# Performance work log

Measured on AMD Instinct MI355X. Metric: run time of the kernel, lower is better.

## Reference

```python
import jax, jax.numpy as jnp
import numpy as np

B, T, V, H, L = 128, 512, 96, 512, 3  # batch, seq_len, n_tokens, n_hidden, n_layers


def setup_inputs() -> dict:
    key = jax.random.key(0)
    ks = jax.random.split(key, 16)
    k = 1.0 / np.sqrt(H)  # PyTorch LSTM/Linear uniform init bound

    def u(kk, shape):
        return jax.random.uniform(kk, shape, jnp.float32, -k, k)

    return {
        "x": jax.random.normal(ks[0], (B, T, V), jnp.float32),
        "h0": jnp.zeros((L, B, H), jnp.float32),
        "c0": jnp.zeros((L, B, H), jnp.float32),
        # layer 0 (input dim V), layers 1-2 (input dim H); gate order i,f,g,o
        "W_ih0": u(ks[1], (4 * H, V)), "W_hh0": u(ks[2], (4 * H, H)),
        "b_ih0": u(ks[3], (4 * H,)), "b_hh0": u(ks[4], (4 * H,)),
        "W_ih1": u(ks[5], (4 * H, H)), "W_hh1": u(ks[6], (4 * H, H)),
        "b_ih1": u(ks[7], (4 * H,)), "b_hh1": u(ks[8], (4 * H,)),
        "W_ih2": u(ks[9], (4 * H, H)), "W_hh2": u(ks[10], (4 * H, H)),
        "b_ih2": u(ks[11], (4 * H,)), "b_hh2": u(ks[12], (4 * H,)),
        "W_fc": u(ks[13], (V, H)), "b_fc": u(ks[14], (V,)),
    }


def _lstm_layer(x, h0, c0, W_ih, W_hh, b_ih, b_hh):
    # Precompute input-to-gate GEMM for the whole sequence: [B,T,4H]
    xg = jnp.einsum('btd,gd->btg', x, W_ih) + b_ih + b_hh

    def step(carry, xg_t):
        h, c = carry
        g = xg_t + h @ W_hh.T  # [B,4H]
        i, f, gg, o = jnp.split(g, 4, axis=-1)
        c = jax.nn.sigmoid(f) * c + jax.nn.sigmoid(i) * jnp.tanh(gg)
        h = jax.nn.sigmoid(o) * jnp.tanh(c)
        return (h, c), h

    (hT, cT), ys = jax.lax.scan(step, (h0, c0), jnp.swapaxes(xg, 0, 1))
    return jnp.swapaxes(ys, 0, 1), hT, cT  # [B,T,H], [B,H], [B,H]


def reference(x, h0, c0, W_ih0, W_hh0, b_ih0, b_hh0, W_ih1, W_hh1, b_ih1, b_hh1,
              W_ih2, W_hh2, b_ih2, b_hh2, W_fc, b_fc):
    params = [(W_ih0, W_hh0, b_ih0, b_hh0),
              (W_ih1, W_hh1, b_ih1, b_hh1),
              (W_ih2, W_hh2, b_ih2, b_hh2)]
    out = x
    hs, cs = [], []
    for l, (Wi, Wh, bi, bh) in enumerate(params):
        out, hT, cT = _lstm_layer(out, h0[l], c0[l], Wi, Wh, bi, bh)
        hs.append(hT)
        cs.append(cT)
    # dropout (inter-layer and post-LSTM) is identity in eval/deterministic mode
    logits = jnp.einsum('bth,vh->btv', out, W_fc) + b_fc  # [B,T,V]
    return logits.reshape(-1, V), jnp.stack(hs), jnp.stack(cs)
```

## Files before the change

### kernel.cpp

```cpp
#include <hip/hip_runtime.h>

#define Bb 128
#define Tt 512
#define Vv 96
#define Hh 512
#define OUT_H 6291456
#define OUT_C 6488064

typedef _Float16 f16x4 __attribute__((ext_vector_type(4)));
typedef _Float16 f16x8 __attribute__((ext_vector_type(8)));
typedef float f32x4 __attribute__((ext_vector_type(4)));

struct KP {
  const float *x, *h0, *c0;
  const float *Wih0, *Whh0, *bih0, *bhh0;
  const float *Wih1, *Whh1, *bih1, *bhh1;
  const float *Wih2, *Whh2, *bih2, *bhh2;
  const float *Wfc, *bfc;
  float* out;
  unsigned* flags;
  float* fbias;
  _Float16* wimg;
  _Float16* wfc;
  _Float16* xb;
  _Float16* hbuf;
};

__device__ __forceinline__ float sigf(float x) { return 1.f / (1.f + __expf(-x)); }

__device__ __forceinline__ void st_dc_u32(unsigned* p, unsigned v) {
  __hip_atomic_store(p, v, __ATOMIC_RELAXED, __HIP_MEMORY_SCOPE_AGENT);
}

__device__ __forceinline__ void wait2(unsigned* flags, int w1, int t1, int w2, int t2) {
  unsigned* p1 = flags + w1;
  unsigned* p2 = flags + w2;
  int g = 0;
  for (;;) {
    int v1 = (int)__hip_atomic_load(p1, __ATOMIC_RELAXED, __HIP_MEMORY_SCOPE_AGENT);
    int v2 = (int)__hip_atomic_load(p2, __ATOMIC_RELAXED, __HIP_MEMORY_SCOPE_AGENT);
    if (__all(v1 >= t1 && v2 >= t2)) break;
    if (++g > 30000) break;
    if (g < 64) __builtin_amdgcn_s_sleep(2);
    else        __builtin_amdgcn_s_sleep(8);
  }
}

template <int KS>
__device__ __forceinline__ void load_pl(const _Float16* __restrict__ p, f16x4 (&av)[KS]) {
#pragma unroll
  for (int i = 0; i < KS; ++i) av[i] = *(const f16x4*)(p + i * 16);
}

template <int KS, int NF>
__device__ __forceinline__ void mma_swz(const f16x4 (&av)[KS], const _Float16* ldsb,
                                        int kb, int l15, int l4, f32x4 (&acc)[NF]) {
#pragma unroll
  for (int i = 0; i < KS; ++i) {
#pragma unroll
    for (int n = 0; n < NF; ++n) {
      const int gr = n * 16 + l15;
      const int idx = ((gr << 9) + kb + i * 16 + (l4 << 2)) ^ ((gr & 7) << 3);
      f16x4 bv = *(const f16x4*)(ldsb + idx);
      acc[n] = __builtin_amdgcn_mfma_f32_16x16x16f16(av[i], bv, acc[n], 0, 0, 0);
    }
  }
}

__global__ __launch_bounds__(256) void prologue_kernel(KP A) {
  const int tid = threadIdx.x, bid = blockIdx.x;
  const int gt = bid * 256 + tid, gn = 98 * 256;
  for (int i = gt; i < Bb * Tt * Vv; i += gn) A.xb[i] = (_Float16)A.x[i];
  for (int i = gt; i < 3 * Bb * Hh; i += gn) {
    int l = i >> 16, b = (i >> 9) & 127, col = i & 511;
    int half = b >> 6, bl = b & 63;
    A.hbuf[(size_t)((l * 2 + half) * 32 + 31) * 32768 + bl * 512 + col] = (_Float16)A.h0[i];
  }
  for (int i = gt; i < 3 * 2048; i += gn) {
    int l = i >> 11, cc = i & 2047;
    const float* bi = (l == 0) ? A.bih0 : (l == 1) ? A.bih1 : A.bih2;
    const float* bh = (l == 0) ? A.bhh0 : (l == 1) ? A.bhh1 : A.bhh2;
    A.fbias[i] = bi[cc] + bh[cc];
  }
  for (int i = gt; i < Vv; i += gn) A.fbias[3 * 2048 + i] = A.bfc[i];

  if (bid < 96) {
    const int l = bid >> 5, c = bid & 31;
    _Float16* img = A.wimg + (size_t)bid * 65536;
    const float* Wh = (l == 0) ? A.Whh0 : (l == 1) ? A.Whh1 : A.Whh2;
    for (int e = tid; e < 64 * 512; e += 256) {
      int r = e >> 9, k = e & 511;
      float v = Wh[((r >> 4) * 512 + c * 16 + (r & 15)) * Hh + k];
      img[(r * 512 + k) ^ ((r & 7) << 3)] = (_Float16)v;
    }
    if (l == 0) {
      for (int e = tid; e < 64 * 96; e += 256) {
        int r = e / 96, k = e - r * 96;
        img[32768 + r * 112 + k] = (_Float16)A.Wih0[((r >> 4) * 512 + c * 16 + (r & 15)) * Vv + k];
      }
    } else {
      const float* Wi = (l == 1) ? A.Wih1 : A.Wih2;
      for (int e = tid; e < 64 * 512; e += 256) {
        int r = e >> 9, k = e & 511;
        float v = Wi[((r >> 4) * 512 + c * 16 + (r & 15)) * Hh + k];
        img[32768 + ((r * 512 + k) ^ ((r & 7) << 3))] = (_Float16)v;
      }
    }
  } else {
    const int r0 = (bid - 96) * 48;
    for (int e = tid; e < 48 * 512; e += 256) {
      int r = r0 + (e >> 9), k = e & 511;
      A.wfc[(r * 512 + k) ^ ((r & 7) << 3)] = (_Float16)A.Wfc[r * 512 + k];
    }
  }
}

__global__ __launch_bounds__(512, 2) void lstm_persist(KP A) {
  __shared__ _Float16 wlds[65536];
  __shared__ float redx[6144];
  const int tid = threadIdx.x, bid = blockIdx.x;
  const int lane = tid & 63, w = tid >> 6;
  const int l15 = lane & 15, l4 = lane >> 4;
  const int mf = w & 3, kh = w >> 2;
  unsigned* flags = A.flags;

  __builtin_amdgcn_fence(__ATOMIC_ACQUIRE, "agent");

  const bool isfc = (bid >= 192);
  const int l = isfc ? 2 : (bid >> 6);
  const int half = isfc ? (bid - 192) : ((bid >> 5) & 1);
  const int c = isfc ? 0 : (bid & 31);
  const int grp = isfc ? 6 : (l * 2 + half);

  {
    const f16x8* src = isfc ? (const f16x8*)A.wfc
                            : (const f16x8*)(A.wimg + (size_t)(l * 32 + c) * 65536);
    f16x8* dst = (f16x8*)wlds;
    const int cnt = isfc ? 6144 : 8192;
    for (int e = tid; e < cnt; e += 512) dst[e] = src[e];
  }

  int w1, w2, off1, off2;
  if (!isfc) {
    w1 = grp * 32 + (lane & 31); off1 = 0;
    if (lane < 32) {
      if (l > 0) { w2 = (grp - 2) * 32 + lane; off2 = 1; }
      else       { w2 = w1; off2 = 0; }
    } else {
      if (l < 2) { w2 = (grp + 2) * 32 + (lane - 32); off2 = -31; }
      else       { w2 = 6 * 32 + half; off2 = -31; }
    }
  } else {
    w1 = (4 + half) * 32 + (lane & 31); off1 = 1;
    w2 = w1; off2 = 1;
  }

  const int arow = mf * 16 + l15;
  const int kb = kh * 256;

  if (!isfc) {
    float biasr[4], creg[4];
#pragma unroll
    for (int n = 0; n < 4; ++n) biasr[n] = A.fbias[l * 2048 + n * 512 + c * 16 + l15];
#pragma unroll
    for (int q = 0; q < 4; ++q)
      creg[q] = A.c0[(size_t)l * 65536 + (half * 64 + mf * 16 + (l4 << 2) + q) * 512 + c * 16 + l15];
    __syncthreads();

    for (int t = 0; t < Tt; ++t) {
      if (tid < 64) wait2(flags, w1, t + off1, w2, t + off2);
      __syncthreads();

      const _Float16* hpv = A.hbuf + (size_t)(grp * 32 + ((t - 1) & 31)) * 32768
                            + arow * 512 + kb + (l4 << 2);
      f32x4 acc[4] = {};
      if (l == 0) {
        f16x4 a2[16];
        load_pl<16>(hpv, a2);
        f16x4 ax[3];
        const _Float16* xp = A.xb + ((size_t)(half * 64 + arow) * 512 + t) * 96
                             + kh * 48 + (l4 << 2);
#pragma unroll
        for (int i = 0; i < 3; ++i) ax[i] = *(const f16x4*)(xp + i * 16);
#pragma unroll
        for (int i = 0; i < 3; ++i)
#pragma unroll
          for (int n = 0; n < 4; ++n) {
            const int gr = n * 16 + l15;
            f16x4 bv = *(const f16x4*)(wlds + 32768 + gr * 112 + kh * 48 + i * 16 + (l4 << 2));
            acc[n] = __builtin_amdgcn_mfma_f32_16x16x16f16(ax[i], bv, acc[n], 0, 0, 0);
          }
        mma_swz<16, 4>(a2, wlds, kb, l15, l4, acc);
      } else {
        const _Float16* hin = A.hbuf + (size_t)((grp - 2) * 32 + (t & 31)) * 32768
                              + arow * 512 + kb + (l4 << 2);
        f16x4 a1[16], a2[16];
        load_pl<16>(hin, a1);
        load_pl<16>(hpv, a2);
        mma_swz<16, 4>(a1, wlds + 32768, kb, l15, l4, acc);
        mma_swz<16, 4>(a2, wlds, kb, l15, l4, acc);
      }

      if (kh == 1) {
#pragma unroll
        for (int n = 0; n < 4; ++n)
          *(f32x4*)&redx[(mf * 4 + n) * 256 + l15 * 16 + (l4 << 2)] = acc[n];
      }
      __syncthreads();
      if (kh == 0) {
#pragma unroll
        for (int n = 0; n < 4; ++n)
          acc[n] += *(const f32x4*)&redx[(mf * 4 + n) * 256 + l15 * 16 + (l4 << 2)];
        _Float16* rp = A.hbuf + (size_t)(grp * 32 + (t & 31)) * 32768;
#pragma unroll
        for (int q = 0; q < 4; ++q) {
          const int bl = mf * 16 + (l4 << 2) + q;
          float gi = acc[0][q] + biasr[0];
          float gf = acc[1][q] + biasr[1];
          float gg = acc[2][q] + biasr[2];
          float go = acc[3][q] + biasr[3];
          float iv = sigf(gi), fv = sigf(gf), gv = tanhf(gg), ov = sigf(go);
          float cn = fv * creg[q] + iv * gv;
          creg[q] = cn;
          float hv = ov * tanhf(cn);
          union { _Float16 h; unsigned short u; } cvt; cvt.h = (_Float16)hv;
          unsigned hb = cvt.u, ob = (unsigned)__shfl_xor((int)hb, 1, 64);
          if ((l15 & 1) == 0)
            st_dc_u32((unsigned*)(rp + bl * 512 + c * 16 + l15), hb | (ob << 16));
          if (t == Tt - 1) {
            A.out[OUT_H + (l * Bb + half * 64 + bl) * 512 + c * 16 + l15] = hv;
            A.out[OUT_C + (l * Bb + half * 64 + bl) * 512 + c * 16 + l15] = cn;
          }
        }
      }
      __syncthreads();
      if (tid == 0) st_dc_u32(&flags[grp * 32 + c], (unsigned)(t + 1));
    }
  } else {
    float biasr[6];
#pragma unroll
    for (int n = 0; n < 6; ++n) biasr[n] = A.fbias[6144 + n * 16 + l15];
    __syncthreads();

    for (int t = 0; t < Tt; ++t) {
      if (tid < 64) wait2(flags, w1, t + off1, w2, t + off2);
      __syncthreads();

      const _Float16* hv2 = A.hbuf + (size_t)((4 + half) * 32 + (t & 31)) * 32768
                            + arow * 512 + kb + (l4 << 2);
      f16x4 a1[16];
      load_pl<16>(hv2, a1);
      f32x4 acc[6] = {};
      mma_swz<16, 6>(a1, wlds, kb, l15, l4, acc);

      if (kh == 1) {
#pragma unroll
        for (int n = 0; n < 6; ++n)
          *(f32x4*)&redx[(mf * 6 + n) * 256 + l15 * 16 + (l4 << 2)] = acc[n];
      }
      __syncthreads();
      if (kh == 0) {
#pragma unroll
        for (int n = 0; n < 6; ++n)
          acc[n] += *(const f32x4*)&redx[(mf * 6 + n) * 256 + l15 * 16 + (l4 << 2)];
#pragma unroll
        for (int q = 0; q < 4; ++q) {
          const int b = half * 64 + mf * 16 + (l4 << 2) + q;
#pragma unroll
          for (int n = 0; n < 6; ++n)
            A.out[((size_t)b * 512 + t) * 96 + n * 16 + l15] = acc[n][q] + biasr[n];
        }
      }
      __syncthreads();
      if (tid == 0) st_dc_u32(&flags[6 * 32 + half], (unsigned)(t + 1));
    }
  }
}

extern "C" void kernel_launch(void* const* d_in, const int* in_sizes, int n_in,
                              void* d_out, int out_size, void* d_ws, size_t ws_size,
                              hipStream_t stream) {
  char* base = (char*)d_ws;
  KP a;
  a.x    = (const float*)d_in[0];
  a.h0   = (const float*)d_in[1];
  a.c0   = (const float*)d_in[2];
  a.Wih0 = (const float*)d_in[3];  a.Whh0 = (const float*)d_in[4];
  a.bih0 = (const float*)d_in[5];  a.bhh0 = (const float*)d_in[6];
  a.Wih1 = (const float*)d_in[7];  a.Whh1 = (const float*)d_in[8];
  a.bih1 = (const float*)d_in[9];  a.bhh1 = (const float*)d_in[10];
  a.Wih2 = (const float*)d_in[11]; a.Whh2 = (const float*)d_in[12];
  a.bih2 = (const float*)d_in[13]; a.bhh2 = (const float*)d_in[14];
  a.Wfc  = (const float*)d_in[15]; a.bfc  = (const float*)d_in[16];
  a.out  = (float*)d_out;
  a.flags = (unsigned*)base;
  a.fbias = (float*)(base + 1024);
  a.wimg  = (_Float16*)(base + 26624);
  a.wfc   = (_Float16*)(base + 12609536);
  a.xb    = (_Float16*)(base + 12707840);
  a.hbuf  = (_Float16*)(base + 25290752);

  hipError_t err = hipMemsetAsync(a.flags, 0, 1024, stream);
  (void)err;
  hipLaunchKernelGGL(prologue_kernel, dim3(98), dim3(256), 0, stream, a);
  hipLaunchKernelGGL(lstm_persist, dim3(194), dim3(512), 0, stream, a);
}
```

Measured before the change: 5.766 ms.

## Retile recurrent MFMA work to 2x2 warp tiles with new LDS swizzle

```diff
diff --git a/kernel.cpp b/kernel.cpp
--- a/kernel.cpp
+++ b/kernel.cpp
@@ -42,27 +42,32 @@
     if (__all(v1 >= t1 && v2 >= t2)) break;
     if (++g > 30000) break;
     if (g < 64) __builtin_amdgcn_s_sleep(2);
-    else        __builtin_amdgcn_s_sleep(8);
+    else        __builtin_amdgcn_s_sleep(4);
   }
 }
 
 template <int KS>
-__device__ __forceinline__ void load_pl(const _Float16* __restrict__ p, f16x4 (&av)[KS]) {
-#pragma unroll
-  for (int i = 0; i < KS; ++i) av[i] = *(const f16x4*)(p + i * 16);
+__device__ __forceinline__ void load2(const _Float16* __restrict__ p, f16x4 (&av)[2][KS]) {
+#pragma unroll
+  for (int m = 0; m < 2; ++m)
+#pragma unroll
+    for (int i = 0; i < KS; ++i)
+      av[m][i] = *(const f16x4*)(p + m * 16 * 512 + i * 16);
 }
 
 template <int KS, int NF>
-__device__ __forceinline__ void mma_swz(const f16x4 (&av)[KS], const _Float16* ldsb,
-                                        int kb, int l15, int l4, f32x4 (&acc)[NF]) {
+__device__ __forceinline__ void mma2(const f16x4 (&av)[2][KS], const _Float16* ldsb,
+                                     int kb, int nbase, int l15, int l4,
+                                     f32x4 (&acc)[2][NF]) {
 #pragma unroll
   for (int i = 0; i < KS; ++i) {
 #pragma unroll
     for (int n = 0; n < NF; ++n) {
-      const int gr = n * 16 + l15;
-      const int idx = ((gr << 9) + kb + i * 16 + (l4 << 2)) ^ ((gr & 7) << 3);
+      const int gr = (nbase + n) * 16 + l15;
+      const int idx = ((gr << 9) + kb + i * 16 + (l4 << 2)) ^ ((gr & 15) << 2);
       f16x4 bv = *(const f16x4*)(ldsb + idx);
-      acc[n] = __builtin_amdgcn_mfma_f32_16x16x16f16(av[i], bv, acc[n], 0, 0, 0);
+      acc[0][n] = __builtin_amdgcn_mfma_f32_16x16x16f16(av[0][i], bv, acc[0][n], 0, 0, 0);
+      acc[1][n] = __builtin_amdgcn_mfma_f32_16x16x16f16(av[1][i], bv, acc[1][n], 0, 0, 0);
     }
   }
 }
@@ -91,7 +96,7 @@
     for (int e = tid; e < 64 * 512; e += 256) {
       int r = e >> 9, k = e & 511;
       float v = Wh[((r >> 4) * 512 + c * 16 + (r & 15)) * Hh + k];
-      img[(r * 512 + k) ^ ((r & 7) << 3)] = (_Float16)v;
+      img[(r * 512 + k) ^ ((r & 15) << 2)] = (_Float16)v;
     }
     if (l == 0) {
       for (int e = tid; e < 64 * 96; e += 256) {
@@ -103,14 +108,14 @@
       for (int e = tid; e < 64 * 512; e += 256) {
         int r = e >> 9, k = e & 511;
         float v = Wi[((r >> 4) * 512 + c * 16 + (r & 15)) * Hh + k];
-        img[32768 + ((r * 512 + k) ^ ((r & 7) << 3))] = (_Float16)v;
+        img[32768 + ((r * 512 + k) ^ ((r & 15) << 2))] = (_Float16)v;
       }
     }
   } else {
     const int r0 = (bid - 96) * 48;
     for (int e = tid; e < 48 * 512; e += 256) {
       int r = r0 + (e >> 9), k = e & 511;
-      A.wfc[(r * 512 + k) ^ ((r & 7) << 3)] = (_Float16)A.Wfc[r * 512 + k];
+      A.wfc[(r * 512 + k) ^ ((r & 15) << 2)] = (_Float16)A.Wfc[r * 512 + k];
     }
   }
 }
@@ -121,7 +126,7 @@
   const int tid = threadIdx.x, bid = blockIdx.x;
   const int lane = tid & 63, w = tid >> 6;
   const int l15 = lane & 15, l4 = lane >> 4;
-  const int mf = w & 3, kh = w >> 2;
+  const int mf = w & 1, nf = (w >> 1) & 1, kh = w >> 2;
   unsigned* flags = A.flags;
 
   __builtin_amdgcn_fence(__ATOMIC_ACQUIRE, "agent");
@@ -155,121 +160,155 @@
     w2 = w1; off2 = 1;
   }
 
-  const int arow = mf * 16 + l15;
   const int kb = kh * 256;
+  const int abase = (mf * 32 + l15) * 512 + kb + (l4 << 2);
 
   if (!isfc) {
-    float biasr[4], creg[4];
+    float biasr[4];
 #pragma unroll
     for (int n = 0; n < 4; ++n) biasr[n] = A.fbias[l * 2048 + n * 512 + c * 16 + l15];
-#pragma unroll
-    for (int q = 0; q < 4; ++q)
-      creg[q] = A.c0[(size_t)l * 65536 + (half * 64 + mf * 16 + (l4 << 2) + q) * 512 + c * 16 + l15];
+    float creg[2][4];
+    if (w < 2) {
+#pragma unroll
+      for (int m = 0; m < 2; ++m)
+#pragma unroll
+        for (int q = 0; q < 4; ++q)
+          creg[m][q] = A.c0[(size_t)l * 65536 + (half * 64 + mf * 32 + m * 16 + (l4 << 2) + q) * 512 + c * 16 + l15];
+    }
     __syncthreads();
 
     for (int t = 0; t < Tt; ++t) {
       if (tid < 64) wait2(flags, w1, t + off1, w2, t + off2);
       __syncthreads();
 
-      const _Float16* hpv = A.hbuf + (size_t)(grp * 32 + ((t - 1) & 31)) * 32768
-                            + arow * 512 + kb + (l4 << 2);
-      f32x4 acc[4] = {};
+      const _Float16* hpv = A.hbuf + (size_t)(grp * 32 + ((t - 1) & 31)) * 32768 + abase;
+      f32x4 acc[2][2] = {};
       if (l == 0) {
-        f16x4 a2[16];
-        load_pl<16>(hpv, a2);
-        f16x4 ax[3];
-        const _Float16* xp = A.xb + ((size_t)(half * 64 + arow) * 512 + t) * 96
-                             + kh * 48 + (l4 << 2);
-#pragma unroll
-        for (int i = 0; i < 3; ++i) ax[i] = *(const f16x4*)(xp + i * 16);
+        f16x4 ah[2][16];
+        load2<16>(hpv, ah);
+        f16x4 ax[2][3];
+#pragma unroll
+        for (int m = 0; m < 2; ++m) {
+          const _Float16* xp = A.xb + ((size_t)(half * 64 + mf * 32 + m * 16 + l15) * 512 + t) * 96
+                               + kh * 48 + (l4 << 2);
+#pragma unroll
+          for (int i = 0; i < 3; ++i) ax[m][i] = *(const f16x4*)(xp + i * 16);
+        }
 #pragma unroll
         for (int i = 0; i < 3; ++i)
 #pragma unroll
-          for (int n = 0; n < 4; ++n) {
-            const int gr = n * 16 + l15;
+          for (int n = 0; n < 2; ++n) {
+            const int gr = (nf * 2 + n) * 16 + l15;
             f16x4 bv = *(const f16x4*)(wlds + 32768 + gr * 112 + kh * 48 + i * 16 + (l4 << 2));
-            acc[n] = __builtin_amdgcn_mfma_f32_16x16x16f16(ax[i], bv, acc[n], 0, 0, 0);
+            acc[0][n] = __builtin_amdgcn_mfma_f32_16x16x16f16(ax[0][i], bv, acc[0][n], 0, 0, 0);
+            acc[1][n] = __builtin_amdgcn_mfma_f32_16x16x16f16(ax[1][i], bv, acc[1][n], 0, 0, 0);
           }
-        mma_swz<16, 4>(a2, wlds, kb, l15, l4, acc);
+        mma2<16, 2>(ah, wlds, kb, nf * 2, l15, l4, acc);
       } else {
-        const _Float16* hin = A.hbuf + (size_t)((grp - 2) * 32 + (t & 31)) * 32768
-                              + arow * 512 + kb + (l4 << 2);
-        f16x4 a1[16], a2[16];
-        load_pl<16>(hin, a1);
-        load_pl<16>(hpv, a2);
-        mma_swz<16, 4>(a1, wlds + 32768, kb, l15, l4, acc);
-        mma_swz<16, 4>(a2, wlds, kb, l15, l4, acc);
-      }
-
-      if (kh == 1) {
-#pragma unroll
-        for (int n = 0; n < 4; ++n)
-          *(f32x4*)&redx[(mf * 4 + n) * 256 + l15 * 16 + (l4 << 2)] = acc[n];
-      }
-      __syncthreads();
-      if (kh == 0) {
-#pragma unroll
-        for (int n = 0; n < 4; ++n)
-          acc[n] += *(const f32x4*)&redx[(mf * 4 + n) * 256 + l15 * 16 + (l4 << 2)];
+        const _Float16* hin = A.hbuf + (size_t)((grp - 2) * 32 + (t & 31)) * 32768 + abase;
+        f16x4 ai[2][16], ah[2][16];
+        load2<16>(hin, ai);
+        load2<16>(hpv, ah);
+        mma2<16, 2>(ai, wlds + 32768, kb, nf * 2, l15, l4, acc);
+        mma2<16, 2>(ah, wlds, kb, nf * 2, l15, l4, acc);
+      }
+
+      if (kh) {
+#pragma unroll
+        for (int m = 0; m < 2; ++m)
+#pragma unroll
+          for (int n = 0; n < 2; ++n)
+#pragma unroll
+            for (int q = 0; q < 4; ++q)
+              redx[((mf * 2 + m) * 4 + nf * 2 + n) * 256 + ((l4 << 2) + q) * 16 + l15] = acc[m][n][q];
+      }
+      __syncthreads();
+      if (!kh) {
+#pragma unroll
+        for (int m = 0; m < 2; ++m)
+#pragma unroll
+          for (int n = 0; n < 2; ++n)
+#pragma unroll
+            for (int q = 0; q < 4; ++q)
+              acc[m][n][q] += redx[((mf * 2 + m) * 4 + nf * 2 + n) * 256 + ((l4 << 2) + q) * 16 + l15];
+        if (nf) {
+#pragma unroll
+          for (int m = 0; m < 2; ++m)
+#pragma unroll
+            for (int n = 0; n < 2; ++n)
+#pragma unroll
+              for (int q = 0; q < 4; ++q)
+                redx[4096 + ((mf * 2 + m) * 2 + n) * 256 + ((l4 << 2) + q) * 16 + l15] = acc[m][n][q];
+        }
+      }
+      __syncthreads();
+      if (w < 2) {
         _Float16* rp = A.hbuf + (size_t)(grp * 32 + (t & 31)) * 32768;
 #pragma unroll
-        for (int q = 0; q < 4; ++q) {
-          const int bl = mf * 16 + (l4 << 2) + q;
-          float gi = acc[0][q] + biasr[0];
-          float gf = acc[1][q] + biasr[1];
-          float gg = acc[2][q] + biasr[2];
-          float go = acc[3][q] + biasr[3];
-          float iv = sigf(gi), fv = sigf(gf), gv = tanhf(gg), ov = sigf(go);
-          float cn = fv * creg[q] + iv * gv;
-          creg[q] = cn;
-          float hv = ov * tanhf(cn);
-          union { _Float16 h; unsigned short u; } cvt; cvt.h = (_Float16)hv;
-          unsigned hb = cvt.u, ob = (unsigned)__shfl_xor((int)hb, 1, 64);
-          if ((l15 & 1) == 0)
-            st_dc_u32((unsigned*)(rp + bl * 512 + c * 16 + l15), hb | (ob << 16));
-          if (t == Tt - 1) {
-            A.out[OUT_H + (l * Bb + half * 64 + bl) * 512 + c * 16 + l15] = hv;
-            A.out[OUT_C + (l * Bb + half * 64 + bl) * 512 + c * 16 + l15] = cn;
+        for (int m = 0; m < 2; ++m)
+#pragma unroll
+          for (int q = 0; q < 4; ++q) {
+            const int bl = mf * 32 + m * 16 + (l4 << 2) + q;
+            float gi = acc[m][0][q] + biasr[0];
+            float gf = acc[m][1][q] + biasr[1];
+            float gg = redx[4096 + ((mf * 2 + m) * 2 + 0) * 256 + ((l4 << 2) + q) * 16 + l15] + biasr[2];
+            float go = redx[4096 + ((mf * 2 + m) * 2 + 1) * 256 + ((l4 << 2) + q) * 16 + l15] + biasr[3];
+            float iv = sigf(gi), fv = sigf(gf), gv = tanhf(gg), ov = sigf(go);
+            float cn = fv * creg[m][q] + iv * gv;
+            creg[m][q] = cn;
+            float hv = ov * tanhf(cn);
+            union { _Float16 h; unsigned short u; } cvt; cvt.h = (_Float16)hv;
+            unsigned hb = cvt.u, ob = (unsigned)__shfl_xor((int)hb, 1, 64);
+            if ((l15 & 1) == 0)
+              st_dc_u32((unsigned*)(rp + bl * 512 + c * 16 + l15), hb | (ob << 16));
+            if (t == Tt - 1) {
+              A.out[OUT_H + (l * Bb + half * 64 + bl) * 512 + c * 16 + l15] = hv;
+              A.out[OUT_C + (l * Bb + half * 64 + bl) * 512 + c * 16 + l15] = cn;
+            }
           }
-        }
       }
       __syncthreads();
       if (tid == 0) st_dc_u32(&flags[grp * 32 + c], (unsigned)(t + 1));
     }
   } else {
-    float biasr[6];
-#pragma unroll
-    for (int n = 0; n < 6; ++n) biasr[n] = A.fbias[6144 + n * 16 + l15];
+    float biasr[3];
+#pragma unroll
+    for (int n = 0; n < 3; ++n) biasr[n] = A.fbias[3 * 2048 + (nf * 3 + n) * 16 + l15];
     __syncthreads();
 
     for (int t = 0; t < Tt; ++t) {
       if (tid < 64) wait2(flags, w1, t + off1, w2, t + off2);
       __syncthreads();
 
-      const _Float16* hv2 = A.hbuf + (size_t)((4 + half) * 32 + (t & 31)) * 32768
-                            + arow * 512 + kb + (l4 << 2);
-      f16x4 a1[16];
-      load_pl<16>(hv2, a1);
-      f32x4 acc[6] = {};
-      mma_swz<16, 6>(a1, wlds, kb, l15, l4, acc);
-
-      if (kh == 1) {
-#pragma unroll
-        for (int n = 0; n < 6; ++n)
-          *(f32x4*)&redx[(mf * 6 + n) * 256 + l15 * 16 + (l4 << 2)] = acc[n];
-      }
-      __syncthreads();
-      if (kh == 0) {
-#pragma unroll
-        for (int n = 0; n < 6; ++n)
-          acc[n] += *(const f32x4*)&redx[(mf * 6 + n) * 256 + l15 * 16 + (l4 << 2)];
-#pragma unroll
-        for (int q = 0; q < 4; ++q) {
-          const int b = half * 64 + mf * 16 + (l4 << 2) + q;
-#pragma unroll
-          for (int n = 0; n < 6; ++n)
-            A.out[((size_t)b * 512 + t) * 96 + n * 16 + l15] = acc[n][q] + biasr[n];
-        }
+      const _Float16* hv2 = A.hbuf + (size_t)((4 + half) * 32 + (t & 31)) * 32768 + abase;
+      f16x4 a1[2][16];
+      load2<16>(hv2, a1);
+      f32x4 acc[2][3] = {};
+      mma2<16, 3>(a1, wlds, kb, nf * 3, l15, l4, acc);
+
+      if (kh) {
+#pragma unroll
+        for (int m = 0; m < 2; ++m)
+#pragma unroll
+          for (int n = 0; n < 3; ++n)
+#pragma unroll
+            for (int q = 0; q < 4; ++q)
+              redx[((mf * 2 + m) * 6 + nf * 3 + n) * 256 + ((l4 << 2) + q) * 16 + l15] = acc[m][n][q];
+      }
+      __syncthreads();
+      if (!kh) {
+#pragma unroll
+        for (int m = 0; m < 2; ++m)
+#pragma unroll
+          for (int q = 0; q < 4; ++q) {
+            const int b = half * 64 + mf * 32 + m * 16 + (l4 << 2) + q;
+#pragma unroll
+            for (int n = 0; n < 3; ++n) {
+              float v = acc[m][n][q]
+                      + redx[((mf * 2 + m) * 6 + nf * 3 + n) * 256 + ((l4 << 2) + q) * 16 + l15];
+              A.out[((size_t)b * 512 + t) * 96 + (nf * 3 + n) * 16 + l15] = v + biasr[n];
+            }
+          }
       }
       __syncthreads();
       if (tid == 0) st_dc_u32(&flags[6 * 32 + half], (unsigned)(t + 1));
```

Result: slower. 9.765 ms (+69.4%).
